# Kernel optimization log

Hardware: AMD Instinct MI355X
Metric: run time of the kernel (lower is better)

Reference implementation:

```python
import jax, jax.numpy as jnp
import numpy as np

EPS = 1e-15  # 0.1 ** 15 in the original


def _mi_table(T):
    # Mutual information of a joint-probability table T [nx, ny]
    P_x = jnp.sum(T, axis=1)  # [nx]
    P_y = jnp.sum(T, axis=0)  # [ny]
    T_xy = P_x[:, None] * P_y[None, :]  # outer product [nx, ny]
    mi = jnp.sum(T * (jnp.log((T + EPS) / (T_xy + EPS)) / jnp.log(jnp.float32(2.0))))
    return mi


def setup_inputs() -> dict:
    key = jax.random.key(0)
    k1, k2 = jax.random.split(key)
    N_ins, N_att, K = 16384, 8192, 64
    Ur = jax.random.uniform(k1, (N_ins, K), dtype=jnp.float32)
    Uc = jax.random.uniform(k2, (N_att, K), dtype=jnp.float32)
    return {"Ur": Ur, "Uc": Uc, "nclu_row": K, "nclu_col": K}


def reference(Ur, Uc, nclu_row, nclu_col):
    # joint probability table  [N_ins, N_att]
    T = Ur @ Uc.T
    T = T / jnp.sum(T)

    v1 = jnp.argmax(Ur, axis=1)  # hard row-cluster ids  [N_ins]
    v2 = jnp.argmax(Uc, axis=1)  # hard col-cluster ids  [N_att]

    # Reduce_Table: segment-sum rows then columns (replaces looped mask+concat)
    T_r = jax.ops.segment_sum(T, v1, num_segments=nclu_row)          # [nclu_row, N_att]
    T_rr = jax.ops.segment_sum(T_r.T, v2, num_segments=nclu_col).T  # [nclu_row, nclu_col]

    mi_org = _mi_table(T)
    mi_red = _mi_table(T_rr)

    loss = jnp.log(1.0 + jnp.abs(1.0 - mi_red / mi_org))
    return loss
```

## Files before the change

kernel.cpp:

```cpp
#include <hip/hip_runtime.h>
#include <hip/hip_bf16.h>

#define N_INS 16384
#define N_ATT 8192
#define KDIM  64

typedef __attribute__((ext_vector_type(8))) short bf16x8;
typedef __attribute__((ext_vector_type(4))) float f32x4;

#define OFF_UCB    0
#define OFF_CPR    1048576
#define OFF_CPC    1064960
#define OFF_ASEG   1073152
#define OFF_BSEG   1138688
#define OFF_GACC   1204224
#define OFF_TK     1204992

#define NBLK_SEG   96
#define NBLK_U     96
#define NBLK_HEAVY 2048
#define NBLK_K2    (NBLK_SEG + NBLK_U + NBLK_HEAVY)

__device__ __forceinline__ unsigned short f2bf(float x) {
    unsigned u = __float_as_uint(x);
    u = (u + 0x7FFFu + ((u >> 16) & 1u)) >> 16;
    return (unsigned short)u;
}

__device__ __forceinline__ float wave_red(float v) {
#pragma unroll
    for (int o = 32; o > 0; o >>= 1) v += __shfl_down(v, o, 64);
    return v;
}

__global__ __launch_bounds__(256)
void k_prep(const float* __restrict__ Ur, const float* __restrict__ Uc,
            float* __restrict__ cpr, float* __restrict__ cpc,
            unsigned short* __restrict__ Ucb,
            float* __restrict__ Aseg, float* __restrict__ Bseg,
            double* __restrict__ Gacc, unsigned* __restrict__ tickets) {
    __shared__ float cs2[256];
    int blk = blockIdx.x, tid = threadIdx.x;
    if (blk < 128) {
        int gid = blk * 256 + tid;
        for (int c = gid; c < N_ATT * 8; c += 32768) {
            int t = c >> 7, o = c & 127;
            int q, m;
            if (o < 64) { q = o >> 4; m = o & 15; }
            else        { q = 4 + ((o - 64) >> 4); m = (o - 64) & 15; }
            int r = t * 16 + m;
            const float4* src = (const float4*)(Uc + (size_t)r * 64 + q * 8);
            float4 x0 = src[0], x1 = src[1];
            uint4 v;
            v.x = (unsigned)f2bf(x0.x) | ((unsigned)f2bf(x0.y) << 16);
            v.y = (unsigned)f2bf(x0.z) | ((unsigned)f2bf(x0.w) << 16);
            v.z = (unsigned)f2bf(x1.x) | ((unsigned)f2bf(x1.y) << 16);
            v.w = (unsigned)f2bf(x1.z) | ((unsigned)f2bf(x1.w) << 16);
            *(uint4*)((unsigned char*)Ucb + (size_t)c * 16) = v;
        }
        return;
    }
    if (blk == 224) {
        float4 z4 = {0.f, 0.f, 0.f, 0.f};
        for (int i = tid; i < 4096; i += 256) ((float4*)Aseg)[i] = z4;
        for (int i = tid; i < 4096; i += 256) ((float4*)Bseg)[i] = z4;
        if (tid < 96) Gacc[tid] = 0.0;
        if (tid < 64) { tickets[tid] = 0u; tickets[64 + tid] = 0u;
                        tickets[128 + tid] = 0u; tickets[192 + tid] = 0u; }
        if (tid < 16) tickets[256 + tid] = 0u;
        return;
    }
    bool isUr = blk < 192;
    int b = isUr ? (blk - 128) : (blk - 192);
    const float* base = (isUr ? Ur : Uc) + (size_t)b * 256 * KDIM;
    float* dst = (isUr ? cpr : cpc) + b * 64;
    int col = tid & 63, r0 = tid >> 6;
    float s = 0.f;
    for (int r = r0; r < 256; r += 4) s += base[r * KDIM + col];
    cs2[tid] = s;
    __syncthreads();
    if (tid < 64) dst[tid] = cs2[tid] + cs2[tid + 64] + cs2[tid + 128] + cs2[tid + 192];
}

__global__ __launch_bounds__(256)
void k_main(const float* __restrict__ Ur, const float* __restrict__ Uc,
            const unsigned char* __restrict__ Ucb,
            const float* __restrict__ cpr, const float* __restrict__ cpc,
            float* __restrict__ Aseg, float* __restrict__ Bseg,
            double* __restrict__ Gacc, unsigned* __restrict__ tickets,
            float* __restrict__ out) {
    __shared__ __align__(16) unsigned char smem[17408];
    __shared__ int flagS;
    int tid = threadIdx.x, blk = blockIdx.x;
    int wvi = tid >> 6, lane = tid & 63;

    if (blk < NBLK_SEG) {
        float* Part = (float*)smem;
        int*   bins = (int*)(smem + 16384);
        bool isUr = blk < 64;
        int b = isUr ? blk : (blk - 64);
        const float* M = isUr ? Ur : Uc;
        float* Seg = (isUr ? Aseg : Bseg) + ((b & 3) << 12);
        int base_row = b * 256;
        for (int i = tid; i < 4096; i += 256) Part[i] = 0.f;
        __syncthreads();
        {
            const float* rp = M + (size_t)(base_row + tid) * KDIM;
            float best = -1e30f; int bidx = 0;
#pragma unroll
            for (int k = 0; k < 64; k += 4) {
                float4 v = *(const float4*)(rp + k);
                if (v.x > best) { best = v.x; bidx = k; }
                if (v.y > best) { best = v.y; bidx = k + 1; }
                if (v.z > best) { best = v.z; bidx = k + 2; }
                if (v.w > best) { best = v.w; bidx = k + 3; }
            }
            bins[tid] = bidx;
        }
        __syncthreads();
        {
            int r0 = wvi * 64;
            const float* Mb = M + (size_t)(base_row + r0) * 64 + lane;
#pragma unroll 4
            for (int r = 0; r < 64; ++r) {
                int bb = bins[r0 + r];
                float val = Mb[(size_t)r * 64];
                atomicAdd(&Part[bb * 64 + lane], val);
            }
        }
        __syncthreads();
        for (int i = tid; i < 4096; i += 256)
            atomicAdd(&Seg[i], Part[i]);
    } else if (blk < NBLK_SEG + NBLK_U) {
        float* wv = (float*)smem;
        bool isUr = blk < (NBLK_SEG + 64);
        int b = isUr ? (blk - NBLK_SEG) : (blk - NBLK_SEG - 64);
        const float* M = isUr ? Ur : Uc;
        int base_row = b * 256;
        if (tid < 64) {
            const float* cpw = isUr ? cpc : cpr;
            int nbw = isUr ? 32 : 64;
            float s = 0.f;
            for (int p = 0; p < nbw; ++p) s += cpw[p * 64 + tid];
            wv[tid] = s;
        }
        __syncthreads();
        const float* rp = M + (size_t)(base_row + tid) * KDIM;
        float u = 0.f;
#pragma unroll
        for (int k = 0; k < 64; k += 4) {
            float4 v = *(const float4*)(rp + k);
            u += v.x * wv[k] + v.y * wv[k + 1] + v.z * wv[k + 2] + v.w * wv[k + 3];
        }
        float pw = wave_red(u * __log2f(u));
        if (lane == 0)
            atomicAdd(&Gacc[(isUr ? 64 : 80) + (b & 15)], (double)pw);
    } else {
        float* gshW = (float*)smem;
        int hb = blk - NBLK_SEG - NBLK_U;
        int quad = lane >> 4, m = lane & 15;
        int rb = hb & 127, cc = hb >> 7;
        int row0 = rb * 128 + wvi * 32;
        bf16x8 a[2][2];
#pragma unroll
        for (int t = 0; t < 2; ++t) {
            int ridx = row0 + t * 16 + m;
            const float* rp = Ur + (size_t)ridx * 64 + quad * 8;
#pragma unroll
            for (int h = 0; h < 2; ++h) {
                const float* rph = rp + h * 32;
                float4 x0 = *(const float4*)rph;
                float4 x1 = *(const float4*)(rph + 4);
                bf16x8 f;
                f[0] = (short)f2bf(x0.x); f[1] = (short)f2bf(x0.y);
                f[2] = (short)f2bf(x0.z); f[3] = (short)f2bf(x0.w);
                f[4] = (short)f2bf(x1.x); f[5] = (short)f2bf(x1.y);
                f[6] = (short)f2bf(x1.z); f[7] = (short)f2bf(x1.w);
                a[t][h] = f;
            }
        }
        const unsigned char* gB = Ucb + (size_t)(cc * 32) * 2048;
        int loff = lane * 16;
        float g0 = 0.f, g1 = 0.f, g2 = 0.f, g3 = 0.f;
        bf16x8 n00 = *(const bf16x8*)(gB + loff);
        bf16x8 n01 = *(const bf16x8*)(gB + 1024 + loff);
        bf16x8 n10 = *(const bf16x8*)(gB + 2048 + loff);
        bf16x8 n11 = *(const bf16x8*)(gB + 3072 + loff);
#pragma unroll 1
        for (int ch = 0; ch < 16; ++ch) {
            bf16x8 c00 = n00, c01 = n01, c10 = n10, c11 = n11;
            if (ch < 15) {
                const unsigned char* nb = gB + (size_t)(ch + 1) * 4096;
                n00 = *(const bf16x8*)(nb + loff);
                n01 = *(const bf16x8*)(nb + 1024 + loff);
                n10 = *(const bf16x8*)(nb + 2048 + loff);
                n11 = *(const bf16x8*)(nb + 3072 + loff);
            }
            f32x4 acc00 = {0.f,0.f,0.f,0.f}, acc01 = {0.f,0.f,0.f,0.f};
            f32x4 acc10 = {0.f,0.f,0.f,0.f}, acc11 = {0.f,0.f,0.f,0.f};
            acc00 = __builtin_amdgcn_mfma_f32_16x16x32_bf16(a[0][0], c00, acc00, 0, 0, 0);
            acc00 = __builtin_amdgcn_mfma_f32_16x16x32_bf16(a[0][1], c01, acc00, 0, 0, 0);
            acc10 = __builtin_amdgcn_mfma_f32_16x16x32_bf16(a[1][0], c00, acc10, 0, 0, 0);
            acc10 = __builtin_amdgcn_mfma_f32_16x16x32_bf16(a[1][1], c01, acc10, 0, 0, 0);
            acc01 = __builtin_amdgcn_mfma_f32_16x16x32_bf16(a[0][0], c10, acc01, 0, 0, 0);
            acc01 = __builtin_amdgcn_mfma_f32_16x16x32_bf16(a[0][1], c11, acc01, 0, 0, 0);
            acc11 = __builtin_amdgcn_mfma_f32_16x16x32_bf16(a[1][0], c10, acc11, 0, 0, 0);
            acc11 = __builtin_amdgcn_mfma_f32_16x16x32_bf16(a[1][1], c11, acc11, 0, 0, 0);
#pragma unroll
            for (int e = 0; e < 4; ++e) {
                float d0 = acc00[e]; g0 += d0 * __log2f(d0);
                float d1 = acc01[e]; g1 += d1 * __log2f(d1);
                float d2 = acc10[e]; g2 += d2 * __log2f(d2);
                float d3 = acc11[e]; g3 += d3 * __log2f(d3);
            }
        }
        float gw = wave_red((g0 + g1) + (g2 + g3));
        if (lane == 0) gshW[wvi] = gw;
        __syncthreads();
        if (tid == 0) {
            float gs = gshW[0] + gshW[1] + gshW[2] + gshW[3];
            atomicAdd(&Gacc[hb & 63], (double)gs);
        }
    }

    __builtin_amdgcn_s_waitcnt(0);
    __syncthreads();
    if (tid == 0) {
        flagS = 0;
        unsigned old = atomicAdd(&tickets[(blk & 15) << 4], 1u);
        if (old == (NBLK_K2 / 16) - 1) {
            unsigned old2 = atomicAdd(&tickets[256], 1u);
            flagS = (old2 == 15u);
        }
    }
    __syncthreads();
    if (!flagS) return;

    for (int i = tid; i < 4096; i += 256) {
        Aseg[i] += Aseg[i + 4096] + Aseg[i + 8192] + Aseg[i + 12288];
        Bseg[i] += Bseg[i + 4096] + Bseg[i + 8192] + Bseg[i + 12288];
    }
    __syncthreads();
    float*  Prx = (float*)smem;
    float*  Pry = (float*)(smem + 256);
    double* sc  = (double*)(smem + 512);
    double* red = (double*)(smem + 1024);
    if (tid < 64) {
        double sa = 0.0, sb = 0.0;
        for (int p = 0; p < 64; ++p) sa += (double)cpr[p * 64 + tid];
        for (int p = 0; p < 32; ++p) sb += (double)cpc[p * 64 + tid];
        red[tid] = sa * sb;
        Prx[tid] = 0.f; Pry[tid] = 0.f;
    }
    __syncthreads();
    if (tid == 0) {
        double s = 0.0;
        for (int k = 0; k < 64; ++k) s += red[k];
        sc[0] = s;
        double gg = 0.0;
        for (int k = 0; k < 64; ++k) gg += Gacc[k];
        sc[1] = gg;
    } else if (tid == 1) {
        double s = 0.0;
        for (int k = 64; k < 80; ++k) s += Gacc[k];
        sc[2] = s;
    } else if (tid == 2) {
        double s = 0.0;
        for (int k = 80; k < 96; ++k) s += Gacc[k];
        sc[3] = s;
    }
    __syncthreads();
    double S = sc[0];
    int p = tid >> 2, q0 = (tid & 3) * 16;
    float tloc[16];
    {
        float prow_sum = 0.f;
        for (int qi = 0; qi < 16; ++qi) {
            int q = q0 + qi;
            double s = 0.0;
            for (int k = 0; k < 64; ++k)
                s += (double)Aseg[p * 64 + k] * (double)Bseg[q * 64 + k];
            float t = (float)(s / S);
            tloc[qi] = t;
            prow_sum += t;
            atomicAdd(&Pry[q], t);
        }
        atomicAdd(&Prx[p], prow_sum);
    }
    __syncthreads();
    {
        const double EPSd = 1e-15;
        double part = 0.0;
        for (int qi = 0; qi < 16; ++qi) {
            double t = (double)tloc[qi];
            double txy = (double)Prx[p] * (double)Pry[q0 + qi];
            part += t * log((t + EPSd) / (txy + EPSd));
        }
        red[tid] = part;
    }
    __syncthreads();
    for (int s2 = 128; s2 > 0; s2 >>= 1) {
        if (tid < s2) red[tid] += red[tid + s2];
        __syncthreads();
    }
    if (tid == 0) {
        const double inv_ln2 = 1.4426950408889634;
        double mi_red = red[0] * inv_ln2;
        double G = sc[1], Uu = sc[2], Vv = sc[3];
        double log2S = log(S) * inv_ln2;
        double mi_org = G / S + log2S - (Uu + Vv) / S;
        double loss = log(1.0 + fabs(1.0 - mi_red / mi_org));
        out[0] = (float)loss;
    }
}

extern "C" void kernel_launch(void* const* d_in, const int* in_sizes, int n_in,
                              void* d_out, int out_size, void* d_ws, size_t ws_size,
                              hipStream_t stream) {
    const float* Ur = (const float*)d_in[0];
    const float* Uc = (const float*)d_in[1];
    float* out = (float*)d_out;
    char* ws = (char*)d_ws;
    unsigned short* Ucb = (unsigned short*)(ws + OFF_UCB);
    float* cpr   = (float*)(ws + OFF_CPR);
    float* cpc   = (float*)(ws + OFF_CPC);
    float* Aseg  = (float*)(ws + OFF_ASEG);
    float* Bseg  = (float*)(ws + OFF_BSEG);
    double* Gacc = (double*)(ws + OFF_GACC);
    unsigned* tickets = (unsigned*)(ws + OFF_TK);

    k_prep<<<225, 256, 0, stream>>>(Ur, Uc, cpr, cpc, Ucb, Aseg, Bseg, Gacc, tickets);
    k_main<<<NBLK_K2, 256, 0, stream>>>(Ur, Uc, (const unsigned char*)Ucb,
                                        cpr, cpc, Aseg, Bseg, Gacc, tickets, out);
}
```

Baseline: 161.7 us.

## Fuse row-marginal entropy blocks into segment-sum blocks via wave-level argmax

The separate block group that computed u*log2(u) for each row is removed. Its work is folded into the segment-sum blocks, which now use a wave-wide shuffle max and ballot to find each row's argmax and a shuffle reduction for the weighted dot product. This removes a second pass over Ur and Uc and 96 blocks from the launch, at the cost of two extra 6-step shuffle reductions per row in the segment blocks. The Ucb conversion loop is also reorganised so reads are linear and the tile permutation moves to the write side. Ties resolve to the lowest index through ffs, which matches the previous strict-greater comparison.

```diff
diff --git a/kernel.cpp b/kernel.cpp
--- a/kernel.cpp
+++ b/kernel.cpp
@@ -17,9 +17,8 @@
 #define OFF_TK     1204992
 
 #define NBLK_SEG   96
-#define NBLK_U     96
 #define NBLK_HEAVY 2048
-#define NBLK_K2    (NBLK_SEG + NBLK_U + NBLK_HEAVY)
+#define NBLK_K2    (NBLK_SEG + NBLK_HEAVY)
 
 __device__ __forceinline__ unsigned short f2bf(float x) {
     unsigned u = __float_as_uint(x);
@@ -44,19 +43,17 @@
     if (blk < 128) {
         int gid = blk * 256 + tid;
         for (int c = gid; c < N_ATT * 8; c += 32768) {
-            int t = c >> 7, o = c & 127;
-            int q, m;
-            if (o < 64) { q = o >> 4; m = o & 15; }
-            else        { q = 4 + ((o - 64) >> 4); m = (o - 64) & 15; }
-            int r = t * 16 + m;
-            const float4* src = (const float4*)(Uc + (size_t)r * 64 + q * 8);
-            float4 x0 = src[0], x1 = src[1];
+            int r = c >> 3, q = c & 7;
+            const float* src = Uc + (size_t)r * 64 + q * 8;
+            float4 x0 = ((const float4*)src)[0], x1 = ((const float4*)src)[1];
             uint4 v;
             v.x = (unsigned)f2bf(x0.x) | ((unsigned)f2bf(x0.y) << 16);
             v.y = (unsigned)f2bf(x0.z) | ((unsigned)f2bf(x0.w) << 16);
             v.z = (unsigned)f2bf(x1.x) | ((unsigned)f2bf(x1.y) << 16);
             v.w = (unsigned)f2bf(x1.z) | ((unsigned)f2bf(x1.w) << 16);
-            *(uint4*)((unsigned char*)Ucb + (size_t)c * 16) = v;
+            int t = r >> 4, m = r & 15;
+            int o = (q < 4) ? (q * 16 + m) : (64 + (q - 4) * 16 + m);
+            *(uint4*)((unsigned char*)Ucb + ((size_t)t * 128 + o) * 16) = v;
         }
         return;
     }
@@ -89,75 +86,53 @@
             float* __restrict__ Aseg, float* __restrict__ Bseg,
             double* __restrict__ Gacc, unsigned* __restrict__ tickets,
             float* __restrict__ out) {
-    __shared__ __align__(16) unsigned char smem[17408];
+    __shared__ __align__(16) unsigned char smem[16640];
     __shared__ int flagS;
     int tid = threadIdx.x, blk = blockIdx.x;
     int wvi = tid >> 6, lane = tid & 63;
 
     if (blk < NBLK_SEG) {
         float* Part = (float*)smem;
-        int*   bins = (int*)(smem + 16384);
+        float* wvs  = (float*)(smem + 16384);
         bool isUr = blk < 64;
         int b = isUr ? blk : (blk - 64);
         const float* M = isUr ? Ur : Uc;
         float* Seg = (isUr ? Aseg : Bseg) + ((b & 3) << 12);
-        int base_row = b * 256;
-        for (int i = tid; i < 4096; i += 256) Part[i] = 0.f;
-        __syncthreads();
-        {
-            const float* rp = M + (size_t)(base_row + tid) * KDIM;
-            float best = -1e30f; int bidx = 0;
-#pragma unroll
-            for (int k = 0; k < 64; k += 4) {
-                float4 v = *(const float4*)(rp + k);
-                if (v.x > best) { best = v.x; bidx = k; }
-                if (v.y > best) { best = v.y; bidx = k + 1; }
-                if (v.z > best) { best = v.z; bidx = k + 2; }
-                if (v.w > best) { best = v.w; bidx = k + 3; }
-            }
-            bins[tid] = bidx;
-        }
-        __syncthreads();
-        {
-            int r0 = wvi * 64;
-            const float* Mb = M + (size_t)(base_row + r0) * 64 + lane;
-#pragma unroll 4
-            for (int r = 0; r < 64; ++r) {
-                int bb = bins[r0 + r];
-                float val = Mb[(size_t)r * 64];
-                atomicAdd(&Part[bb * 64 + lane], val);
-            }
-        }
-        __syncthreads();
-        for (int i = tid; i < 4096; i += 256)
-            atomicAdd(&Seg[i], Part[i]);
-    } else if (blk < NBLK_SEG + NBLK_U) {
-        float* wv = (float*)smem;
-        bool isUr = blk < (NBLK_SEG + 64);
-        int b = isUr ? (blk - NBLK_SEG) : (blk - NBLK_SEG - 64);
-        const float* M = isUr ? Ur : Uc;
         int base_row = b * 256;
         if (tid < 64) {
             const float* cpw = isUr ? cpc : cpr;
             int nbw = isUr ? 32 : 64;
             float s = 0.f;
             for (int p = 0; p < nbw; ++p) s += cpw[p * 64 + tid];
-            wv[tid] = s;
-        }
+            wvs[tid] = s;
+        }
+        for (int i = tid; i < 4096; i += 256) Part[i] = 0.f;
         __syncthreads();
-        const float* rp = M + (size_t)(base_row + tid) * KDIM;
-        float u = 0.f;
-#pragma unroll
-        for (int k = 0; k < 64; k += 4) {
-            float4 v = *(const float4*)(rp + k);
-            u += v.x * wv[k] + v.y * wv[k + 1] + v.z * wv[k + 2] + v.w * wv[k + 3];
-        }
-        float pw = wave_red(u * __log2f(u));
+        float wv = wvs[lane];
+        float ulog = 0.f;
+        const float* Mb = M + (size_t)(base_row + wvi * 64) * 64 + lane;
+#pragma unroll 4
+        for (int r = 0; r < 64; ++r) {
+            float v = Mb[(size_t)r * 64];
+            float mx = v;
+#pragma unroll
+            for (int o = 32; o > 0; o >>= 1) mx = fmaxf(mx, __shfl_xor(mx, o, 64));
+            unsigned long long msk = __ballot(v == mx);
+            int idx = __ffsll((unsigned long long)msk) - 1;
+            float pd = v * wv;
+#pragma unroll
+            for (int o = 32; o > 0; o >>= 1) pd += __shfl_xor(pd, o, 64);
+            if (lane == 0) ulog += pd * __log2f(pd);
+            atomicAdd(&Part[idx * 64 + lane], v);
+        }
         if (lane == 0)
-            atomicAdd(&Gacc[(isUr ? 64 : 80) + (b & 15)], (double)pw);
+            atomicAdd(&Gacc[(isUr ? 64 : 80) + (b & 15)], (double)ulog);
+        __syncthreads();
+        for (int i = tid; i < 4096; i += 256)
+            atomicAdd(&Seg[i], Part[i]);
     } else {
         float* gshW = (float*)smem;
-        int hb = blk - NBLK_SEG - NBLK_U;
+        int hb = blk - NBLK_SEG;
         int quad = lane >> 4, m = lane & 15;
         int rb = hb & 127, cc = hb >> 7;
         int row0 = rb * 128 + wvi * 32;
```

Result: slower. 192.7 us (+19.2%).
